# Optimization experiments

Hardware: AMD Instinct MI355X
Metric: run time of the kernel (lower is better)

Reference implementation:

```python
import jax, jax.numpy as jnp
import numpy as np

N, E, G = 50000, 800000, 64
F_IN, H = 128, 256


def setup_inputs() -> dict:
    key = jax.random.key(0)
    ks = jax.random.split(key, 16)
    s = 0.05
    return {
        "x": jax.random.normal(ks[0], (N, F_IN), jnp.float32),
        "edge_index": jax.random.randint(ks[1], (2, E), 0, N, jnp.int32),
        "batch": jnp.sort(jax.random.randint(ks[2], (N,), 0, G, jnp.int32)),
        "W1": jax.random.normal(ks[3], (F_IN, H), jnp.float32) * s,
        "b1": jnp.zeros((H,), jnp.float32),
        "W2": jax.random.normal(ks[4], (H, H), jnp.float32) * s,
        "b2": jnp.zeros((H,), jnp.float32),
        "W3": jax.random.normal(ks[5], (H, H), jnp.float32) * s,
        "b3": jnp.zeros((H,), jnp.float32),
        "Wc1": jax.random.normal(ks[6], (2 * H, 512), jnp.float32) * s,
        "bc1": jnp.zeros((512,), jnp.float32),
        "Wc2": jax.random.normal(ks[7], (512, 256), jnp.float32) * s,
        "bc2": jnp.zeros((256,), jnp.float32),
        "Wc3": jax.random.normal(ks[8], (256, 5), jnp.float32) * s,
        "bc3": jnp.zeros((5,), jnp.float32),
    }


def _gcn_conv(x, src, dst, dis, W, b):
    # PyG GCNConv: h = x W; out = D^{-1/2}(A+I)D^{-1/2} h + b
    h = x @ W                                        # [N, H]
    coef = (dis[src] * dis[dst])[:, None]            # [E, 1]
    agg = jax.ops.segment_sum(h[src] * coef, dst, num_segments=x.shape[0])
    return agg + h * (dis * dis)[:, None] + b        # self-loop term


def reference(x, edge_index, batch, W1, b1, W2, b2, W3, b3,
              Wc1, bc1, Wc2, bc2, Wc3, bc3):
    src, dst = edge_index[0], edge_index[1]
    # degree with self loops (in-degree at dst, as PyG)
    deg = jax.ops.segment_sum(jnp.ones_like(dst, jnp.float32), dst,
                              num_segments=x.shape[0]) + 1.0
    dis = jax.lax.rsqrt(deg)                         # D^{-1/2}

    h = jax.nn.relu(_gcn_conv(x, src, dst, dis, W1, b1))  # dropout=identity (eval)
    h = jax.nn.relu(_gcn_conv(h, src, dst, dis, W2, b2))
    h = jax.nn.relu(_gcn_conv(h, src, dst, dis, W3, b3))

    # global mean / max pool per graph
    cnt = jax.ops.segment_sum(jnp.ones_like(batch, jnp.float32), batch,
                              num_segments=G)
    x_mean = jax.ops.segment_sum(h, batch, num_segments=G) / jnp.maximum(cnt, 1.0)[:, None]
    x_max = jax.ops.segment_max(h, batch, num_segments=G)
    x_max = jnp.where(cnt[:, None] > 0, x_max, 0.0)  # guard empty segments
    g = jnp.concatenate([x_mean, x_max], axis=1)     # [G, 512]

    g = jax.nn.relu(g @ Wc1 + bc1)
    g = jax.nn.relu(g @ Wc2 + bc2)
    return g @ Wc3 + bc3                             # [G, 5]
```

## Files before the change

kernel.cpp:

```cpp
#include <hip/hip_runtime.h>
#include <cstdint>

#define CDIV(a, b) (((a) + (b) - 1) / (b))

typedef short bf16x8 __attribute__((ext_vector_type(8)));
typedef float f32x4 __attribute__((ext_vector_type(4)));

__device__ inline ushort f2bf_rn(float f) {
    uint32_t u = __float_as_uint(f);
    uint32_t rounding = 0x7FFF + ((u >> 16) & 1);
    return (ushort)((u + rounding) >> 16);
}
__device__ inline float bf2f(ushort h) { return __uint_as_float((uint32_t)h << 16); }

__global__ void k_init(int* __restrict__ degc, int N, float* __restrict__ sumbuf,
                       int* __restrict__ maxbuf, int PB) {
    int i = blockIdx.x * blockDim.x + threadIdx.x;
    if (i < N) degc[i] = 0;
    if (i < PB) { sumbuf[i] = 0.f; maxbuf[i] = 0; }
}

__global__ void k_deg(const int* __restrict__ dst, int E, int* __restrict__ degc) {
    int e = blockIdx.x * blockDim.x + threadIdx.x;
    if (e < E) atomicAdd(&degc[dst[e]], 1);
}

__global__ void k_xsplit(const float* __restrict__ x, int n, ushort* __restrict__ xhi) {
    int i = blockIdx.x * blockDim.x + threadIdx.x;
    if (i < n) xhi[i] = f2bf_rn(x[i]);
}

__global__ void k_scan_partial(const int* __restrict__ degc, int N, int* __restrict__ csum) {
    __shared__ int sm[256];
    int t = threadIdx.x;
    int idx = blockIdx.x * 1024 + t * 4;
    int s = 0;
#pragma unroll
    for (int j = 0; j < 4; ++j)
        if (idx + j < N) s += degc[idx + j];
    sm[t] = s;
    __syncthreads();
    for (int off = 128; off > 0; off >>= 1) {
        if (t < off) sm[t] += sm[t + off];
        __syncthreads();
    }
    if (t == 0) csum[blockIdx.x] = sm[0];
}

__global__ void k_scan_chunks(const int* __restrict__ csum, int nch, int* __restrict__ coff,
                              int* __restrict__ row_ptr, int N, int E) {
    if (threadIdx.x == 0 && blockIdx.x == 0) {
        int run = 0;
        for (int i = 0; i < nch; ++i) { coff[i] = run; run += csum[i]; }
        row_ptr[N] = E;
    }
}

__global__ void k_scan_final(const int* __restrict__ degc, int N, const int* __restrict__ coff,
                             int* __restrict__ row_ptr, int* __restrict__ fill,
                             float* __restrict__ dis) {
    __shared__ int sm[256];
    int t = threadIdx.x;
    int idx = blockIdx.x * 1024 + t * 4;
    int v[4];
    int s = 0;
#pragma unroll
    for (int j = 0; j < 4; ++j) {
        v[j] = (idx + j < N) ? degc[idx + j] : 0;
        s += v[j];
    }
    sm[t] = s;
    __syncthreads();
    for (int off = 1; off < 256; off <<= 1) {
        int x = (t >= off) ? sm[t - off] : 0;
        __syncthreads();
        sm[t] += x;
        __syncthreads();
    }
    int excl = sm[t] - s + coff[blockIdx.x];
#pragma unroll
    for (int j = 0; j < 4; ++j) {
        if (idx + j < N) {
            row_ptr[idx + j] = excl;
            fill[idx + j] = 0;
            dis[idx + j] = rsqrtf((float)v[j] + 1.0f);
            excl += v[j];
        }
    }
}

__global__ void k_fill(const int* __restrict__ src, const int* __restrict__ dst, int E,
                       const int* __restrict__ row_ptr, int* __restrict__ fill,
                       int* __restrict__ esrc) {
    int e = blockIdx.x * blockDim.x + threadIdx.x;
    if (e >= E) return;
    int d = dst[e], s = src[e];
    int pos = row_ptr[d] + atomicAdd(&fill[d], 1);
    esrc[pos] = s;
}

template <int C, bool SELF_F32>
__global__ __launch_bounds__(256) void k_agg(const float* __restrict__ xf,
                                             const ushort* __restrict__ hhi,
                                             const float* __restrict__ dis,
                                             const int* __restrict__ row_ptr,
                                             const int* __restrict__ esrc, int N,
                                             ushort* __restrict__ ohi,
                                             ushort* __restrict__ olo) {
    constexpr int V = C / 64;
    int wave = (blockIdx.x * blockDim.x + threadIdx.x) >> 6;
    int lane = threadIdx.x & 63;
    if (wave >= N) return;
    const int i = wave;
    const float di = dis[i];
    const float dd = di * di;
    float acc[V];
    if constexpr (SELF_F32) {
        const float* xr = xf + (size_t)i * C + lane * V;
        if constexpr (V == 4) {
            float4 v = *reinterpret_cast<const float4*>(xr);
            acc[0] = dd * v.x; acc[1] = dd * v.y; acc[2] = dd * v.z; acc[3] = dd * v.w;
        } else {
            float2 v = *reinterpret_cast<const float2*>(xr);
            acc[0] = dd * v.x; acc[1] = dd * v.y;
        }
    } else {
        size_t sb = (size_t)i * C + lane * V;
        if constexpr (V == 4) {
            ushort4 h = *reinterpret_cast<const ushort4*>(hhi + sb);
            acc[0] = dd * bf2f(h.x); acc[1] = dd * bf2f(h.y);
            acc[2] = dd * bf2f(h.z); acc[3] = dd * bf2f(h.w);
        } else {
            ushort2 h = *reinterpret_cast<const ushort2*>(hhi + sb);
            acc[0] = dd * bf2f(h.x); acc[1] = dd * bf2f(h.y);
        }
    }
    const int p0 = row_ptr[i], p1 = row_ptr[i + 1];
    int p = p0;
    if constexpr (V == 4) {
        for (; p + 8 <= p1; p += 8) {
            int s[8];
            float c[8];
            ushort4 v[8];
#pragma unroll
            for (int j = 0; j < 8; ++j) s[j] = esrc[p + j];
#pragma unroll
            for (int j = 0; j < 8; ++j)
                v[j] = *reinterpret_cast<const ushort4*>(hhi + (size_t)s[j] * C + lane * V);
#pragma unroll
            for (int j = 0; j < 8; ++j) c[j] = dis[s[j]] * di;
#pragma unroll
            for (int j = 0; j < 8; ++j) {
                acc[0] += c[j] * bf2f(v[j].x); acc[1] += c[j] * bf2f(v[j].y);
                acc[2] += c[j] * bf2f(v[j].z); acc[3] += c[j] * bf2f(v[j].w);
            }
        }
        for (; p + 4 <= p1; p += 4) {
            int s0 = esrc[p], s1 = esrc[p + 1], s2 = esrc[p + 2], s3 = esrc[p + 3];
            float c0 = dis[s0] * di, c1 = dis[s1] * di, c2 = dis[s2] * di, c3 = dis[s3] * di;
            ushort4 v0 = *reinterpret_cast<const ushort4*>(hhi + (size_t)s0 * C + lane * V);
            ushort4 v1 = *reinterpret_cast<const ushort4*>(hhi + (size_t)s1 * C + lane * V);
            ushort4 v2 = *reinterpret_cast<const ushort4*>(hhi + (size_t)s2 * C + lane * V);
            ushort4 v3 = *reinterpret_cast<const ushort4*>(hhi + (size_t)s3 * C + lane * V);
            acc[0] += c0 * bf2f(v0.x); acc[1] += c0 * bf2f(v0.y);
            acc[2] += c0 * bf2f(v0.z); acc[3] += c0 * bf2f(v0.w);
            acc[0] += c1 * bf2f(v1.x); acc[1] += c1 * bf2f(v1.y);
            acc[2] += c1 * bf2f(v1.z); acc[3] += c1 * bf2f(v1.w);
            acc[0] += c2 * bf2f(v2.x); acc[1] += c2 * bf2f(v2.y);
            acc[2] += c2 * bf2f(v2.z); acc[3] += c2 * bf2f(v2.w);
            acc[0] += c3 * bf2f(v3.x); acc[1] += c3 * bf2f(v3.y);
            acc[2] += c3 * bf2f(v3.z); acc[3] += c3 * bf2f(v3.w);
        }
        for (; p < p1; ++p) {
            int s = esrc[p];
            float c = dis[s] * di;
            ushort4 v = *reinterpret_cast<const ushort4*>(hhi + (size_t)s * C + lane * V);
            acc[0] += c * bf2f(v.x); acc[1] += c * bf2f(v.y);
            acc[2] += c * bf2f(v.z); acc[3] += c * bf2f(v.w);
        }
    } else {
        for (; p + 8 <= p1; p += 8) {
            int s[8];
            float c[8];
            ushort2 v[8];
#pragma unroll
            for (int j = 0; j < 8; ++j) s[j] = esrc[p + j];
#pragma unroll
            for (int j = 0; j < 8; ++j)
                v[j] = *reinterpret_cast<const ushort2*>(hhi + (size_t)s[j] * C + lane * V);
#pragma unroll
            for (int j = 0; j < 8; ++j) c[j] = dis[s[j]] * di;
#pragma unroll
            for (int j = 0; j < 8; ++j) {
                acc[0] += c[j] * bf2f(v[j].x);
                acc[1] += c[j] * bf2f(v[j].y);
            }
        }
        for (; p < p1; ++p) {
            int s = esrc[p];
            float c = dis[s] * di;
            ushort2 v = *reinterpret_cast<const ushort2*>(hhi + (size_t)s * C + lane * V);
            acc[0] += c * bf2f(v.x); acc[1] += c * bf2f(v.y);
        }
    }
    ushort hi[V], lo[V];
#pragma unroll
    for (int j = 0; j < V; ++j) {
        hi[j] = f2bf_rn(acc[j]);
        lo[j] = f2bf_rn(acc[j] - bf2f(hi[j]));
    }
    size_t ob = (size_t)i * C + lane * V;
    if constexpr (V == 4) {
        *reinterpret_cast<ushort4*>(ohi + ob) = make_ushort4(hi[0], hi[1], hi[2], hi[3]);
        *reinterpret_cast<ushort4*>(olo + ob) = make_ushort4(lo[0], lo[1], lo[2], lo[3]);
    } else {
        *reinterpret_cast<ushort2*>(ohi + ob) = make_ushort2(hi[0], hi[1]);
        *reinterpret_cast<ushort2*>(olo + ob) = make_ushort2(lo[0], lo[1]);
    }
}

__global__ void k_wsplit(const float* __restrict__ W, int K, ushort* __restrict__ Whi,
                         ushort* __restrict__ Wlo) {
    int idx = blockIdx.x * 256 + threadIdx.x;
    if (idx >= K * 256) return;
    int k = idx >> 8, n = idx & 255;
    float v = W[idx];
    ushort hi = f2bf_rn(v);
    ushort lo = f2bf_rn(v - bf2f(hi));
    int ks = k >> 5, r = k & 31;
    int lane = (r >> 3) * 16 + (n & 15);
    int j = r & 7;
    size_t d = (((size_t)ks * 16 + (n >> 4)) * 64 + lane) * 8 + j;
    Whi[d] = hi;
    Wlo[d] = lo;
}

template <int K, bool POOL>
__global__ __launch_bounds__(256) void k_gemm_bf16(const ushort* __restrict__ Ahi,
                                                   const ushort* __restrict__ Alo,
                                                   const ushort* __restrict__ Whi,
                                                   const ushort* __restrict__ Wlo,
                                                   const float* __restrict__ bias, int M,
                                                   ushort* __restrict__ Hhi,
                                                   const int* __restrict__ batch,
                                                   float* __restrict__ sumbuf,
                                                   int* __restrict__ maxbuf) {
    __shared__ ushort Bs[2][2][8][512];
    const int t = threadIdx.x;
    const int w = t >> 6, lane = t & 63;

    const int nwg = (int)gridDim.x;
    const int orig = (int)blockIdx.x;
    const int q = nwg >> 3, r = nwg & 7;
    const int xcd = orig & 7;
    const int swz = (xcd < r ? xcd * (q + 1) : r * (q + 1) + (xcd - r) * q) + (orig >> 3);
    const int bm = (swz >> 1) * 128;
    const int bn = (swz & 1) * 128;
    const int rw = bm + w * 32;

    f32x4 acc[2][8] = {};

    int row0 = min(rw + (lane & 15), M - 1);
    int row1 = min(rw + 16 + (lane & 15), M - 1);
    const int kbase = (lane >> 4) * 8;
    const ushort* pa0h = Ahi + (size_t)row0 * K + kbase;
    const ushort* pa0l = Alo + (size_t)row0 * K + kbase;
    const ushort* pa1h = Ahi + (size_t)row1 * K + kbase;
    const ushort* pa1l = Alo + (size_t)row1 * K + kbase;
    const int nf0 = bn >> 4;
    constexpr int KS = K / 32;

    bf16x8 sbh[2], sbl[2];
    auto loadB = [&](int ks) {
#pragma unroll
        for (int q2 = 0; q2 < 2; ++q2) {
            int nf = (w << 1) | q2;
            size_t widx = (((size_t)ks * 16 + nf0 + nf) * 64 + lane) * 8;
            sbh[q2] = *reinterpret_cast<const bf16x8*>(Whi + widx);
            sbl[q2] = *reinterpret_cast<const bf16x8*>(Wlo + widx);
        }
    };
    auto writeB = [&](int b) {
#pragma unroll
        for (int q2 = 0; q2 < 2; ++q2) {
            int nf = (w << 1) | q2;
            *reinterpret_cast<bf16x8*>(&Bs[b][0][nf][lane * 8]) = sbh[q2];
            *reinterpret_cast<bf16x8*>(&Bs[b][1][nf][lane * 8]) = sbl[q2];
        }
    };

    bf16x8 c0h, c0l, c1h, c1l, n0h, n0l, n1h, n1l;
    auto loadA = [&](int ks, bf16x8& x0h, bf16x8& x0l, bf16x8& x1h, bf16x8& x1l) {
        x0h = *reinterpret_cast<const bf16x8*>(pa0h + ks * 32);
        x0l = *reinterpret_cast<const bf16x8*>(pa0l + ks * 32);
        x1h = *reinterpret_cast<const bf16x8*>(pa1h + ks * 32);
        x1l = *reinterpret_cast<const bf16x8*>(pa1l + ks * 32);
    };

    loadB(0);
    writeB(0);
    loadA(0, c0h, c0l, c1h, c1l);
    if (KS > 1) loadB(1);
    __syncthreads();

#pragma unroll
    for (int ks = 0; ks < KS; ++ks) {
        const int buf = ks & 1;
        if (ks + 1 < KS) loadA(ks + 1, n0h, n0l, n1h, n1l);
#pragma unroll
        for (int nf = 0; nf < 8; ++nf) {
            bf16x8 bh = *reinterpret_cast<const bf16x8*>(&Bs[buf][0][nf][lane * 8]);
            bf16x8 bl = *reinterpret_cast<const bf16x8*>(&Bs[buf][1][nf][lane * 8]);
            acc[0][nf] = __builtin_amdgcn_mfma_f32_16x16x32_bf16(c0h, bh, acc[0][nf], 0, 0, 0);
            acc[0][nf] = __builtin_amdgcn_mfma_f32_16x16x32_bf16(c0h, bl, acc[0][nf], 0, 0, 0);
            acc[0][nf] = __builtin_amdgcn_mfma_f32_16x16x32_bf16(c0l, bh, acc[0][nf], 0, 0, 0);
            acc[1][nf] = __builtin_amdgcn_mfma_f32_16x16x32_bf16(c1h, bh, acc[1][nf], 0, 0, 0);
            acc[1][nf] = __builtin_amdgcn_mfma_f32_16x16x32_bf16(c1h, bl, acc[1][nf], 0, 0, 0);
            acc[1][nf] = __builtin_amdgcn_mfma_f32_16x16x32_bf16(c1l, bh, acc[1][nf], 0, 0, 0);
        }
        if (ks + 1 < KS) {
            writeB(buf ^ 1);
            if (ks + 2 < KS) loadB(ks + 2);
            __syncthreads();
            c0h = n0h; c0l = n0l; c1h = n1h; c1l = n1l;
        }
    }

    const int colq = lane & 15;
    const int rowq = (lane >> 4) * 4;

    if constexpr (!POOL) {
#pragma unroll
        for (int m = 0; m < 2; ++m) {
#pragma unroll
            for (int nf = 0; nf < 8; ++nf) {
                int col = bn + nf * 16 + colq;
                float bia = bias[col];
#pragma unroll
                for (int r2 = 0; r2 < 4; ++r2) {
                    int rr = rw + m * 16 + rowq + r2;
                    if (rr < M) {
                        float v = fmaxf(acc[m][nf][r2] + bia, 0.f);
                        Hhi[(size_t)rr * 256 + col] = f2bf_rn(v);
                    }
                }
            }
        }
    } else {
        int r0 = min(rw + rowq, M - 1);
        int r7 = min(rw + 16 + rowq + 3, M - 1);
        int g0 = batch[r0];
        int g7 = batch[r7];
        int gfirst = __shfl(g0, 0);
        bool uni = __all(g0 == gfirst && g7 == gfirst);
        if (uni) {
#pragma unroll
            for (int nf = 0; nf < 8; ++nf) {
                int col = bn + nf * 16 + colq;
                float bia = bias[col];
                float s = 0.f, mx = 0.f;
#pragma unroll
                for (int m = 0; m < 2; ++m) {
#pragma unroll
                    for (int r2 = 0; r2 < 4; ++r2) {
                        int rr = rw + m * 16 + rowq + r2;
                        float v = fmaxf(acc[m][nf][r2] + bia, 0.f);
                        if (rr < M) { s += v; mx = fmaxf(mx, v); }
                    }
                }
                s += __shfl_xor(s, 16);
                mx = fmaxf(mx, __shfl_xor(mx, 16));
                s += __shfl_xor(s, 32);
                mx = fmaxf(mx, __shfl_xor(mx, 32));
                if ((lane >> 4) == 0) {
                    atomicAdd(&sumbuf[gfirst * 256 + col], s);
                    atomicMax(&maxbuf[gfirst * 256 + col], __float_as_int(mx));
                }
            }
        } else {
#pragma unroll
            for (int nf = 0; nf < 8; ++nf) {
                int col = bn + nf * 16 + colq;
                float bia = bias[col];
#pragma unroll
                for (int m = 0; m < 2; ++m) {
#pragma unroll
                    for (int r2 = 0; r2 < 4; ++r2) {
                        int rr = rw + m * 16 + rowq + r2;
                        if (rr < M) {
                            float v = fmaxf(acc[m][nf][r2] + bia, 0.f);
                            int g = batch[rr];
                            atomicAdd(&sumbuf[g * 256 + col], v);
                            atomicMax(&maxbuf[g * 256 + col], __float_as_int(v));
                        }
                    }
                }
            }
        }
    }
}

__global__ __launch_bounds__(512) void k_head(const float* __restrict__ sumbuf,
                                              const int* __restrict__ maxbuf,
                                              const int* __restrict__ batch, int N,
                                              const float* __restrict__ Wc1,
                                              const float* __restrict__ bc1,
                                              const float* __restrict__ Wc2,
                                              const float* __restrict__ bc2,
                                              const float* __restrict__ Wc3,
                                              const float* __restrict__ bc3,
                                              float* __restrict__ out) {
    __shared__ float gf[512];
    __shared__ float h1[512];
    __shared__ float h2[256];
    __shared__ int cntS;
    const int g = blockIdx.x;
    const int t = threadIdx.x;

    if (t == 0) {
        int lo = 0, hi = N;
        while (lo < hi) { int mid = (lo + hi) >> 1; if (batch[mid] < g) lo = mid + 1; else hi = mid; }
        int s = lo;
        lo = 0; hi = N;
        while (lo < hi) { int mid = (lo + hi) >> 1; if (batch[mid] < g + 1) lo = mid + 1; else hi = mid; }
        cntS = lo - s;
    }
    __syncthreads();
    const int cnt = cntS;
    if (t < 256) {
        float mean = sumbuf[g * 256 + t] / fmaxf((float)cnt, 1.0f);
        float mx = __int_as_float(maxbuf[g * 256 + t]);
        if (cnt == 0) { mean = 0.f; mx = 0.f; }
        gf[t] = mean;
        gf[256 + t] = mx;
    }
    __syncthreads();
    {
        float a0 = 0.f, a1 = 0.f, a2 = 0.f, a3 = 0.f;
        for (int k = 0; k < 512; k += 4) {
            a0 += gf[k + 0] * Wc1[(size_t)(k + 0) * 512 + t];
            a1 += gf[k + 1] * Wc1[(size_t)(k + 1) * 512 + t];
            a2 += gf[k + 2] * Wc1[(size_t)(k + 2) * 512 + t];
            a3 += gf[k + 3] * Wc1[(size_t)(k + 3) * 512 + t];
        }
        h1[t] = fmaxf((a0 + a1) + (a2 + a3) + bc1[t], 0.f);
    }
    __syncthreads();
    if (t < 256) {
        float a0 = 0.f, a1 = 0.f, a2 = 0.f, a3 = 0.f;
        for (int k = 0; k < 512; k += 4) {
            a0 += h1[k + 0] * Wc2[(size_t)(k + 0) * 256 + t];
            a1 += h1[k + 1] * Wc2[(size_t)(k + 1) * 256 + t];
            a2 += h1[k + 2] * Wc2[(size_t)(k + 2) * 256 + t];
            a3 += h1[k + 3] * Wc2[(size_t)(k + 3) * 256 + t];
        }
        h2[t] = fmaxf((a0 + a1) + (a2 + a3) + bc2[t], 0.f);
    }
    __syncthreads();
    if (t < 5) {
        float a = bc3[t];
        for (int k = 0; k < 256; ++k) a += h2[k] * Wc3[(size_t)k * 5 + t];
        out[(size_t)g * 5 + t] = a;
    }
}

extern "C" void kernel_launch(void* const* d_in, const int* in_sizes, int n_in, void* d_out,
                              int out_size, void* d_ws, size_t ws_size, hipStream_t stream) {
    const float* x = (const float*)d_in[0];
    const int* eidx = (const int*)d_in[1];
    const int* batch = (const int*)d_in[2];
    const float* W1 = (const float*)d_in[3];
    const float* b1 = (const float*)d_in[4];
    const float* W2 = (const float*)d_in[5];
    const float* b2 = (const float*)d_in[6];
    const float* W3 = (const float*)d_in[7];
    const float* b3 = (const float*)d_in[8];
    const float* Wc1 = (const float*)d_in[9];
    const float* bc1 = (const float*)d_in[10];
    const float* Wc2 = (const float*)d_in[11];
    const float* bc2 = (const float*)d_in[12];
    const float* Wc3 = (const float*)d_in[13];
    const float* bc3 = (const float*)d_in[14];
    float* out = (float*)d_out;

    const int N = in_sizes[2];
    const int E = in_sizes[1] / 2;
    const int G = out_size / 5;
    const int* src = eidx;
    const int* dst = eidx + E;

    char* p = (char*)d_ws;
    auto alloc = [&](size_t bytes) {
        void* r = (void*)p;
        p += (bytes + 255) & ~(size_t)255;
        return r;
    };
    float* dis = (float*)alloc((size_t)N * 4);
    int* degc = (int*)alloc((size_t)N * 4);
    int* row_ptr = (int*)alloc((size_t)(N + 1) * 4);
    int* fill = (int*)alloc((size_t)N * 4);
    const int nch = CDIV(N, 1024);
    int* csum = (int*)alloc((size_t)nch * 4);
    int* coff = (int*)alloc((size_t)nch * 4);
    int* esrc = (int*)alloc((size_t)E * 4);
    float* sumbuf = (float*)alloc((size_t)G * 256 * 4);
    int* maxbuf = (int*)alloc((size_t)G * 256 * 4);
    ushort* Ahi = (ushort*)alloc((size_t)N * 256 * 2);
    ushort* Alo = (ushort*)alloc((size_t)N * 256 * 2);
    ushort* Hhi = (ushort*)alloc((size_t)N * 256 * 2);
    ushort* Xhi = (ushort*)alloc((size_t)N * 128 * 2);
    ushort* W1hi = (ushort*)alloc((size_t)128 * 256 * 2);
    ushort* W1lo = (ushort*)alloc((size_t)128 * 256 * 2);
    ushort* W2hi = (ushort*)alloc((size_t)256 * 256 * 2);
    ushort* W2lo = (ushort*)alloc((size_t)256 * 256 * 2);
    ushort* W3hi = (ushort*)alloc((size_t)256 * 256 * 2);
    ushort* W3lo = (ushort*)alloc((size_t)256 * 256 * 2);
    (void)ws_size;

    k_init<<<CDIV(N, 256), 256, 0, stream>>>(degc, N, sumbuf, maxbuf, G * 256);

    k_wsplit<<<CDIV(128 * 256, 256), 256, 0, stream>>>(W1, 128, W1hi, W1lo);
    k_wsplit<<<CDIV(256 * 256, 256), 256, 0, stream>>>(W2, 256, W2hi, W2lo);
    k_wsplit<<<CDIV(256 * 256, 256), 256, 0, stream>>>(W3, 256, W3hi, W3lo);
    k_xsplit<<<CDIV(N * 128, 256), 256, 0, stream>>>(x, N * 128, Xhi);

    k_deg<<<CDIV(E, 256), 256, 0, stream>>>(dst, E, degc);
    k_scan_partial<<<nch, 256, 0, stream>>>(degc, N, csum);
    k_scan_chunks<<<1, 64, 0, stream>>>(csum, nch, coff, row_ptr, N, E);
    k_scan_final<<<nch, 256, 0, stream>>>(degc, N, coff, row_ptr, fill, dis);
    k_fill<<<CDIV(E, 256), 256, 0, stream>>>(src, dst, E, row_ptr, fill, esrc);

    const int ggrid = CDIV(N, 128) * 2;

    k_agg<128, true><<<CDIV(N * 64, 256), 256, 0, stream>>>(x, Xhi, dis, row_ptr, esrc, N,
                                                            Ahi, Alo);
    k_gemm_bf16<128, false><<<ggrid, 256, 0, stream>>>(Ahi, Alo, W1hi, W1lo, b1, N, Hhi,
                                                       batch, sumbuf, maxbuf);
    k_agg<256, false><<<CDIV(N * 64, 256), 256, 0, stream>>>(nullptr, Hhi, dis, row_ptr,
                                                             esrc, N, Ahi, Alo);
    k_gemm_bf16<256, false><<<ggrid, 256, 0, stream>>>(Ahi, Alo, W2hi, W2lo, b2, N, Hhi,
                                                       batch, sumbuf, maxbuf);
    k_agg<256, false><<<CDIV(N * 64, 256), 256, 0, stream>>>(nullptr, Hhi, dis, row_ptr,
                                                             esrc, N, Ahi, Alo);
    k_gemm_bf16<256, true><<<ggrid, 256, 0, stream>>>(Ahi, Alo, W3hi, W3lo, b3, N, Hhi,
                                                      batch, sumbuf, maxbuf);

    k_head<<<G, 512, 0, stream>>>(sumbuf, maxbuf, batch, N, Wc1, bc1, Wc2, bc2, Wc3, bc3, out);
}
```

Measured before the change: 434.0 us.

## Store aggregated activations in MFMA fragment layout and deepen A-operand prefetch

The aggregation kernel now writes its hi/lo bf16 outputs in a tiled layout that matches the MFMA A-fragment order. Each lane's 8-element load in the GEMM then comes from a contiguous 512-element block instead of a strided row access. The GEMM prefetches A two k-steps ahead instead of one, and the A buffers are padded to a multiple of 128 rows so the row clamp can be dropped. The gather loop also drops its 8-way unroll in favour of the 4-way loop, adding a 4-way loop for the V==2 path. The costs are higher register pressure from the extra prefetch registers, and the GEMM now reads unwritten padded rows.

```diff
diff --git a/kernel.cpp b/kernel.cpp
--- a/kernel.cpp
+++ b/kernel.cpp
@@ -138,23 +138,6 @@
     const int p0 = row_ptr[i], p1 = row_ptr[i + 1];
     int p = p0;
     if constexpr (V == 4) {
-        for (; p + 8 <= p1; p += 8) {
-            int s[8];
-            float c[8];
-            ushort4 v[8];
-#pragma unroll
-            for (int j = 0; j < 8; ++j) s[j] = esrc[p + j];
-#pragma unroll
-            for (int j = 0; j < 8; ++j)
-                v[j] = *reinterpret_cast<const ushort4*>(hhi + (size_t)s[j] * C + lane * V);
-#pragma unroll
-            for (int j = 0; j < 8; ++j) c[j] = dis[s[j]] * di;
-#pragma unroll
-            for (int j = 0; j < 8; ++j) {
-                acc[0] += c[j] * bf2f(v[j].x); acc[1] += c[j] * bf2f(v[j].y);
-                acc[2] += c[j] * bf2f(v[j].z); acc[3] += c[j] * bf2f(v[j].w);
-            }
-        }
         for (; p + 4 <= p1; p += 4) {
             int s0 = esrc[p], s1 = esrc[p + 1], s2 = esrc[p + 2], s3 = esrc[p + 3];
             float c0 = dis[s0] * di, c1 = dis[s1] * di, c2 = dis[s2] * di, c3 = dis[s3] * di;
@@ -179,22 +162,17 @@
             acc[2] += c * bf2f(v.z); acc[3] += c * bf2f(v.w);
         }
     } else {
-        for (; p + 8 <= p1; p += 8) {
-            int s[8];
-            float c[8];
-            ushort2 v[8];
-#pragma unroll
-            for (int j = 0; j < 8; ++j) s[j] = esrc[p + j];
-#pragma unroll
-            for (int j = 0; j < 8; ++j)
-                v[j] = *reinterpret_cast<const ushort2*>(hhi + (size_t)s[j] * C + lane * V);
-#pragma unroll
-            for (int j = 0; j < 8; ++j) c[j] = dis[s[j]] * di;
-#pragma unroll
-            for (int j = 0; j < 8; ++j) {
-                acc[0] += c[j] * bf2f(v[j].x);
-                acc[1] += c[j] * bf2f(v[j].y);
-            }
+        for (; p + 4 <= p1; p += 4) {
+            int s0 = esrc[p], s1 = esrc[p + 1], s2 = esrc[p + 2], s3 = esrc[p + 3];
+            float c0 = dis[s0] * di, c1 = dis[s1] * di, c2 = dis[s2] * di, c3 = dis[s3] * di;
+            ushort2 v0 = *reinterpret_cast<const ushort2*>(hhi + (size_t)s0 * C + lane * V);
+            ushort2 v1 = *reinterpret_cast<const ushort2*>(hhi + (size_t)s1 * C + lane * V);
+            ushort2 v2 = *reinterpret_cast<const ushort2*>(hhi + (size_t)s2 * C + lane * V);
+            ushort2 v3 = *reinterpret_cast<const ushort2*>(hhi + (size_t)s3 * C + lane * V);
+            acc[0] += c0 * bf2f(v0.x); acc[1] += c0 * bf2f(v0.y);
+            acc[0] += c1 * bf2f(v1.x); acc[1] += c1 * bf2f(v1.y);
+            acc[0] += c2 * bf2f(v2.x); acc[1] += c2 * bf2f(v2.y);
+            acc[0] += c3 * bf2f(v3.x); acc[1] += c3 * bf2f(v3.y);
         }
         for (; p < p1; ++p) {
             int s = esrc[p];
@@ -209,13 +187,15 @@
         hi[j] = f2bf_rn(acc[j]);
         lo[j] = f2bf_rn(acc[j] - bf2f(hi[j]));
     }
-    size_t ob = (size_t)i * C + lane * V;
+    const int c0 = lane * V;
+    size_t fb = ((size_t)(i >> 4) * (C / 32) + (c0 >> 5)) * 512 +
+                (size_t)(((i & 15) + ((c0 >> 3) & 3) * 16) * 8 + (c0 & 7));
     if constexpr (V == 4) {
-        *reinterpret_cast<ushort4*>(ohi + ob) = make_ushort4(hi[0], hi[1], hi[2], hi[3]);
-        *reinterpret_cast<ushort4*>(olo + ob) = make_ushort4(lo[0], lo[1], lo[2], lo[3]);
+        *reinterpret_cast<ushort4*>(ohi + fb) = make_ushort4(hi[0], hi[1], hi[2], hi[3]);
+        *reinterpret_cast<ushort4*>(olo + fb) = make_ushort4(lo[0], lo[1], lo[2], lo[3]);
     } else {
-        *reinterpret_cast<ushort2*>(ohi + ob) = make_ushort2(hi[0], hi[1]);
-        *reinterpret_cast<ushort2*>(olo + ob) = make_ushort2(lo[0], lo[1]);
+        *reinterpret_cast<ushort2*>(ohi + fb) = make_ushort2(hi[0], hi[1]);
+        *reinterpret_cast<ushort2*>(olo + fb) = make_ushort2(lo[0], lo[1]);
     }
 }
 
@@ -248,6 +228,7 @@
     __shared__ ushort Bs[2][2][8][512];
     const int t = threadIdx.x;
     const int w = t >> 6, lane = t & 63;
+    constexpr int KS = K / 32;
 
     const int nwg = (int)gridDim.x;
     const int orig = (int)blockIdx.x;
@@ -260,15 +241,11 @@
 
     f32x4 acc[2][8] = {};
 
-    int row0 = min(rw + (lane & 15), M - 1);
-    int row1 = min(rw + 16 + (lane & 15), M - 1);
-    const int kbase = (lane >> 4) * 8;
-    const ushort* pa0h = Ahi + (size_t)row0 * K + kbase;
-    const ushort* pa0l = Alo + (size_t)row0 * K + kbase;
-    const ushort* pa1h = Ahi + (size_t)row1 * K + kbase;
-    const ushort* pa1l = Alo + (size_t)row1 * K + kbase;
+    const size_t fbase = ((size_t)(rw >> 4) * KS) * 512 + (size_t)lane * 8;
+    const ushort* pa_h = Ahi + fbase;
+    const ushort* pa_l = Alo + fbase;
+    const size_t rb1 = (size_t)KS * 512;
     const int nf0 = bn >> 4;
-    constexpr int KS = K / 32;
 
     bf16x8 sbh[2], sbl[2];
     auto loadB = [&](int ks) {
@@ -289,24 +266,26 @@
         }
     };
 
-    bf16x8 c0h, c0l, c1h, c1l, n0h, n0l, n1h, n1l;
+    bf16x8 c0h, c0l, c1h, c1l, n0h, n0l, n1h, n1l, m0h, m0l, m1h, m1l;
     auto loadA = [&](int ks, bf16x8& x0h, bf16x8& x0l, bf16x8& x1h, bf16x8& x1l) {
-        x0h = *reinterpret_cast<const bf16x8*>(pa0h + ks * 32);
-        x0l = *reinterpret_cast<const bf16x8*>(pa0l + ks * 32);
-        x1h = *reinterpret_cast<const bf16x8*>(pa1h + ks * 32);
-        x1l = *reinterpret_cast<const bf16x8*>(pa1l + ks * 32);
+        size_t o = (size_t)ks * 512;
+        x0h = *reinterpret_cast<const bf16x8*>(pa_h + o);
+        x0l = *reinterpret_cast<const bf16x8*>(pa_l + o);
+        x1h = *reinterpret_cast<const bf16x8*>(pa_h + rb1 + o);
+        x1l = *reinterpret_cast<const bf16x8*>(pa_l + rb1 + o);
     };
 
     loadB(0);
     writeB(0);
     loadA(0, c0h, c0l, c1h, c1l);
+    if (KS > 1) loadA(1, n0h, n0l, n1h, n1l);
     if (KS > 1) loadB(1);
     __syncthreads();
 
 #pragma unroll
     for (int ks = 0; ks < KS; ++ks) {
         const int buf = ks & 1;
-        if (ks + 1 < KS) loadA(ks + 1, n0h, n0l, n1h, n1l);
+        if (ks + 2 < KS) loadA(ks + 2, m0h, m0l, m1h, m1l);
 #pragma unroll
         for (int nf = 0; nf < 8; ++nf) {
             bf16x8 bh = *reinterpret_cast<const bf16x8*>(&Bs[buf][0][nf][lane * 8]);
@@ -323,6 +302,7 @@
             if (ks + 2 < KS) loadB(ks + 2);
             __syncthreads();
             c0h = n0h; c0l = n0l; c1h = n1h; c1l = n1l;
+            n0h = m0h; n0l = m0l; n1h = m1h; n1l = m1l;
         }
     }
 
@@ -488,6 +468,7 @@
     const int G = out_size / 5;
     const int* src = eidx;
     const int* dst = eidx + E;
+    const int Npad = CDIV(N, 128) * 128;
 
     char* p = (char*)d_ws;
     auto alloc = [&](size_t bytes) {
@@ -505,8 +486,8 @@
     int* esrc = (int*)alloc((size_t)E * 4);
     float* sumbuf = (float*)alloc((size_t)G * 256 * 4);
     int* maxbuf = (int*)alloc((size_t)G * 256 * 4);
-    ushort* Ahi = (ushort*)alloc((size_t)N * 256 * 2);
-    ushort* Alo = (ushort*)alloc((size_t)N * 256 * 2);
+    ushort* Ahi = (ushort*)alloc((size_t)Npad * 256 * 2);
+    ushort* Alo = (ushort*)alloc((size_t)Npad * 256 * 2);
     ushort* Hhi = (ushort*)alloc((size_t)N * 256 * 2);
     ushort* Xhi = (ushort*)alloc((size_t)N * 128 * 2);
     ushort* W1hi = (ushort*)alloc((size_t)128 * 256 * 2);
```

Result: slower. 453.3 us (+4.5%).
